# Kernel optimization log

Measured on AMD Instinct MI355X. Metric: run time of the kernel, lower is better.

The kernel has to match this reference:

```python
import jax
import jax.numpy as jnp
from jax import lax
import numpy as np

EPS = 1e-5
CLASS_COUNT = 1000

# conv specs: (out_c, in_c, k, pool_stride)
_SPECS = [(8, 1, 11, 1), (32, 8, 7, 2), (64, 32, 5, 2), (64, 64, 5, 2), (128, 64, 5, 2), (128, 128, 3, 2)]


def _maxpool3(x, stride):
    return lax.reduce_window(x, -jnp.inf, lax.max, (1, 1, 3, 3), (1, 1, stride, stride), 'VALID')


def _block(x, w, gamma, beta, pool_stride):
    # tanh soft-binarized weights (mode=1, w=1)
    wq = jnp.tanh(w)
    y = lax.conv_general_dilated(x, wq, (1, 1), 'VALID', dimension_numbers=('NCHW', 'OIHW', 'NCHW'))
    y = _maxpool3(y, pool_stride)
    # BatchNorm2d in training mode: batch statistics over (N,H,W), biased var
    mu = jnp.mean(y, axis=(0, 2, 3), keepdims=True)
    var = jnp.var(y, axis=(0, 2, 3), keepdims=True)
    y = (y - mu) * lax.rsqrt(var + EPS)
    y = y * gamma.reshape(1, -1, 1, 1) + beta.reshape(1, -1, 1, 1)
    # tanh soft-binarized activation (mode=1, w=1)
    return jnp.tanh(y)


def setup_inputs() -> dict:
    key = jax.random.key(0)
    keys = jax.random.split(key, 8)
    inp = {'x': jax.random.normal(keys[0], (128, 1, 227, 227), dtype=jnp.float32)}
    for i, (oc, ic, k, _) in enumerate(_SPECS):
        fan_in = ic * k * k
        inp[f'w{i+1}'] = jax.random.normal(keys[i + 1], (oc, ic, k, k), dtype=jnp.float32) / np.sqrt(fan_in)
        inp[f'g{i+1}'] = jnp.ones((oc,), dtype=jnp.float32)
        inp[f'b{i+1}'] = jnp.zeros((oc,), dtype=jnp.float32)
    inp['wl'] = jax.random.normal(keys[7], (CLASS_COUNT, 512), dtype=jnp.float32) / np.sqrt(512.0)
    return inp


def reference(x, w1, w2, w3, w4, w5, w6, g1, g2, g3, g4, g5, g6,
              b1, b2, b3, b4, b5, b6, wl):
    ws = (w1, w2, w3, w4, w5, w6)
    gs = (g1, g2, g3, g4, g5, g6)
    bs = (b1, b2, b3, b4, b5, b6)
    for i, (_, _, _, ps) in enumerate(_SPECS):
        x = _block(x, ws[i], gs[i], bs[i], ps)
    # flatten -> BinaryLinear (tanh-binarized weight, no bias)
    x = x.reshape(x.shape[0], -1)  # [B, 512]
    return x @ jnp.tanh(wl).T  # [B, classCount]
```

## Files before the change

kernel.cpp:

```cpp
#include <hip/hip_runtime.h>
#include <hip/hip_bf16.h>
#include <hip/hip_fp16.h>

using bf16 = __hip_bfloat16;
using f16  = _Float16;
using f16x8 = __attribute__((ext_vector_type(8))) _Float16;
using f32x4  = __attribute__((ext_vector_type(4))) float;
typedef unsigned long long u64;

__device__ __forceinline__ float b2f(bf16 v){ return __bfloat162float(v); }
__device__ __forceinline__ bf16 f2b(float v){ return __float2bfloat16(v); }
__device__ __forceinline__ float ldf(const float* p){ return *p; }
__device__ __forceinline__ float ldf(const bf16* p){ return b2f(*p); }
__device__ __forceinline__ float ldf(const __half* p){ return __half2float(*p); }
__device__ __forceinline__ void stf(float* p, float v){ *p = v; }
__device__ __forceinline__ void stf(bf16* p, float v){ *p = f2b(v); }
__device__ __forceinline__ void stf(__half* p, float v){ *p = __float2half(v); }

__device__ __forceinline__ float ftanh(float x){
    float t = __builtin_amdgcn_exp2f(x * 2.8853900817779268f);
    return 1.0f - 2.0f * __builtin_amdgcn_rcpf(t + 1.0f);
}

__device__ __forceinline__ float ld_any(const void* p, int i, int isBf16)
{
    return isBf16 ? b2f(((const bf16*)p)[i]) : ((const float*)p)[i];
}

__device__ __forceinline__ int det_bf(const void* g)
{
    return (*(const unsigned*)g == 0x3F803F80u) ? 1 : 0;
}

__device__ __forceinline__ void bn_pr(const float* __restrict__ sums,
                                      const void* __restrict__ g,
                                      const void* __restrict__ b,
                                      int bf, int C, float inv, int c,
                                      float& sc, float& sh)
{
    float mean = sums[c] * inv;
    float var  = sums[C + c] * inv - mean * mean;
    float rstd = rsqrtf(fmaxf(var, 0.f) + 1e-5f);
    sc = ld_any(g, c, bf) * rstd;
    sh = ld_any(b, c, bf) - mean * sc;
}

__global__ __launch_bounds__(256)
void prep_all(const void* __restrict__ w1, const void* __restrict__ w6,
              const void* __restrict__ wlw, const void* __restrict__ w2,
              const void* __restrict__ w3, const void* __restrict__ w4,
              const void* __restrict__ w5, const void* __restrict__ g1,
              float* __restrict__ wq0, float* __restrict__ wq5,
              float* __restrict__ wlqT, __half* __restrict__ wpk,
              __half* __restrict__ wpk3, __half* __restrict__ wpk4,
              __half* __restrict__ wpk5, int* __restrict__ flag)
{
    const int bf = det_bf(g1);
    const int b = blockIdx.x, t = threadIdx.x;
    if (b == 0 && t == 0) *flag = bf;
    if (b < 4) {
        int i = b * 256 + t;
        if (i < 968) wq0[i] = tanhf(ld_any(w1, i, bf));
    } else if (b < 580) {
        int i = (b - 4) * 256 + t;
        if (i < 147456) wq5[i] = tanhf(ld_any(w6, i, bf));
    } else if (b < 2580) {
        int i = (b - 580) * 256 + t;
        if (i < 512000) {
            int cls = i >> 9, k = i & 511;
            wlqT[k * 1000 + cls] = tanhf(ld_any(wlw, i, bf));
        }
    } else if (b < 2636) {
        int i = (b - 2580) * 256 + t;
        if (i < 14336) {
            int ic  = i & 7;
            int q   = (i >> 3) & 3;
            int col = (i >> 5) & 15;
            int g   = (i >> 9) & 1;
            int khg = (i >> 10) & 1;
            int kw  = i >> 11;
            int kh  = khg * 4 + q;
            int oc  = g * 16 + col;
            __half v = __float2half(0.f);
            if (kh < 7)
                v = __float2half(tanhf(ld_any(w2, (oc * 8 + ic) * 49 + kh * 7 + kw, bf)));
            wpk[i] = v;
        }
    } else if (b < 2836) {
        int i = (b - 2636) * 256 + t;
        if (i < 51200) {
            int tap = i >> 11;
            int g   = (i >> 9) & 3;
            int col = (i >> 5) & 15;
            int icp = i & 31;
            int oc  = g * 16 + col;
            wpk3[i] = __float2half(tanhf(ld_any(w3, (oc * 32 + icp) * 25 + tap, bf)));
        }
    } else if (b < 3236) {
        int i = (b - 2836) * 256 + t;
        if (i < 102400) {
            int step = i >> 11;
            int g    = (i >> 9) & 3;
            int col  = (i >> 5) & 15;
            int icp  = i & 31;
            int icg  = step / 25, tap = step - icg * 25;
            int oc   = g * 16 + col;
            int ic   = icg * 32 + icp;
            wpk4[i] = __float2half(tanhf(ld_any(w4, (oc * 64 + ic) * 25 + tap, bf)));
        }
    } else {
        int i = (b - 3236) * 256 + t;
        if (i < 204800) {
            int step = i >> 12;
            int ocg  = (i >> 11) & 1;
            int g    = (i >> 9) & 3;
            int col  = (i >> 5) & 15;
            int icp  = i & 31;
            int icg  = step / 25, tap = step - icg * 25;
            int oc   = ocg * 64 + g * 16 + col;
            int ic   = icg * 32 + icp;
            wpk5[i] = __float2half(tanhf(ld_any(w5, (oc * 64 + ic) * 25 + tap, bf)));
        }
    }
}

__global__ __launch_bounds__(256)
void b2conv(const __half* __restrict__ A1, const __half* __restrict__ wpk,
            __half* __restrict__ raw, float* __restrict__ sums2,
            const float* __restrict__ sums1, const void* __restrict__ g1,
            const void* __restrict__ b1)
{
    __shared__ __align__(16) char smem[32000];
    __shared__ float s_part[512];
    f16*   xs = (f16*)smem;
    float* pb = (float*)smem;

    const int tid = threadIdx.x;
    const int n   = blockIdx.z;
    const int ty  = blockIdx.x / 15, tx = blockIdx.x - ty * 15;
    const int cy0 = ty * 30, cx0 = tx * 14;

    const int bf1 = det_bf(g1);
    float ssc[8], ssh[8];
    #pragma unroll
    for (int j = 0; j < 8; j++)
        bn_pr(sums1, g1, b1, bf1, 8, 1.f / 5916800.f, j, ssc[j], ssh[j]);

    for (int i = tid; i < 858; i += 256) {
        int r = i / 22, c = i - r * 22;
        int gr = cy0 + r, gc = cx0 + c;
        f16x8 v = (f16x8){0, 0, 0, 0, 0, 0, 0, 0};
        if (gr < 215 && gc < 215)
            v = *(const f16x8*)((const f16*)A1 + ((size_t)(n * 215 + gr) * 215 + gc) * 8);
        f16x8 o;
        #pragma unroll
        for (int j = 0; j < 8; j++)
            o[j] = (f16)ftanh(fmaf((float)v[j], ssc[j], ssh[j]));
        *(f16x8*)(xs + i * 8) = o;
    }
    __syncthreads();

    const int lane = tid & 63, wid = tid >> 6;
    const int col = lane & 15, q = lane >> 4;
    const int arow = q * 22;

    f32x4 acc[8][2];
    #pragma unroll
    for (int f = 0; f < 8; f++)
        #pragma unroll
        for (int g = 0; g < 2; g++)
            acc[f][g] = (f32x4){0.f, 0.f, 0.f, 0.f};

    const f16* wb = (const f16*)wpk + col * 32 + q * 8;
    f16x8 wc0 = *(const f16x8*)(wb);
    f16x8 wc1 = *(const f16x8*)(wb + 512);

    #pragma unroll
    for (int s = 0; s < 14; s++) {
        f16x8 wn0 = wc0, wn1 = wc1;
        if (s < 13) {
            const f16* wn = wb + (s + 1) * 1024;
            wn0 = *(const f16x8*)(wn);
            wn1 = *(const f16x8*)(wn + 512);
        }
        int kw = s >> 1, khg = s & 1;
        int aoffs = arow + khg * 88 + kw;
        #pragma unroll
        for (int f = 0; f < 8; f++) {
            int gi = (wid * 8 + f) * 22 + col + aoffs;
            f16x8 a = *(const f16x8*)(xs + gi * 8);
            acc[f][0] = __builtin_amdgcn_mfma_f32_16x16x32_f16(a, wc0, acc[f][0], 0, 0, 0);
            acc[f][1] = __builtin_amdgcn_mfma_f32_16x16x32_f16(a, wc1, acc[f][1], 0, 0, 0);
        }
        wc0 = wn0; wc1 = wn1;
    }
    __syncthreads();

    for (int h = 0; h < 2; h++) {
        #pragma unroll
        for (int f = 0; f < 8; f++) {
            int cr = wid * 8 + f;
            if (cr < 31)
                *(f32x4*)(pb + col * 500 + cr * 16 + q * 4) = acc[f][h];
        }
        __syncthreads();
        const int ocl = tid >> 4, slot = tid & 15;
        float sm = 0.f, sq = 0.f;
        for (int j = slot; j < 105; j += 16) {
            int py = j / 7, px = j - (j / 7) * 7;
            int gph = ty * 15 + py, gpw = tx * 7 + px;
            if (gph < 104 && gpw < 104) {
                const float* cp = pb + ocl * 500 + (2 * py) * 16 + 2 * px;
                float m = cp[0];
                #pragma unroll
                for (int dy = 0; dy < 3; dy++)
                    #pragma unroll
                    for (int dx = 0; dx < 3; dx++)
                        m = fmaxf(m, cp[dy * 16 + dx]);
                int oc = h * 16 + ocl;
                size_t oidx = ((size_t)(n * 104 + gph) * 104 + gpw) * 32 + oc;
                raw[oidx] = __float2half(m);
                sm += m; sq += m * m;
            }
        }
        s_part[tid] = sm; s_part[256 + tid] = sq;
        __syncthreads();
        if (tid < 16) {
            float a = 0.f, b = 0.f;
            #pragma unroll
            for (int t = 0; t < 16; t++) {
                a += s_part[tid * 16 + t];
                b += s_part[256 + tid * 16 + t];
            }
            atomicAdd(&sums2[h * 16 + tid],      a);
            atomicAdd(&sums2[32 + h * 16 + tid], b);
        }
        __syncthreads();
    }
}

__global__ __launch_bounds__(256)
void b3conv(const __half* __restrict__ A2, const __half* __restrict__ wpk3,
            __half* __restrict__ A3t, float* __restrict__ sums3,
            const float* __restrict__ sums2, const void* __restrict__ g2,
            const void* __restrict__ b2)
{
    __shared__ __align__(16) char smem[32000];
    __shared__ float s_part[512];
    f16*   xs = (f16*)smem;
    float* pb = (float*)smem;

    const int tid = threadIdx.x;
    const int n   = blockIdx.z;
    const int ty  = blockIdx.x / 7, tx = blockIdx.x - ty * 7;
    const int y0  = ty * 14, x0 = tx * 14;

    if (tid < 32) {
        float sc, sh;
        bn_pr(sums2, g2, b2, det_bf(g2), 32, 1.f / 1384448.f, tid, sc, sh);
        s_part[tid] = sc; s_part[32 + tid] = sh;
    }
    __syncthreads();

    for (int i = tid; i < 1600; i += 256) {
        int pos = i >> 2, g8 = i & 3;
        int gy = y0 + pos / 20, gx = x0 + pos % 20;
        f16x8 v = *(const f16x8*)((const f16*)A2 +
                  ((size_t)(n * 104 + gy) * 104 + gx) * 32 + g8 * 8);
        int c0 = g8 * 8;
        f16x8 o;
        #pragma unroll
        for (int j = 0; j < 8; j++)
            o[j] = (f16)ftanh(fmaf((float)v[j], s_part[c0 + j], s_part[32 + c0 + j]));
        *(f16x8*)(xs + pos * 40 + g8 * 8) = o;
    }

    const int lane = tid & 63, wid = tid >> 6;
    const int col = lane & 15, q = lane >> 4;

    f32x4 acc[4][4];
    #pragma unroll
    for (int f = 0; f < 4; f++)
        #pragma unroll
        for (int g = 0; g < 4; g++)
            acc[f][g] = (f32x4){0.f, 0.f, 0.f, 0.f};

    const f16* wb = (const f16*)wpk3 + col * 32 + q * 8;
    f16x8 w[4];
    #pragma unroll
    for (int g = 0; g < 4; g++)
        w[g] = *(const f16x8*)(wb + g * 512);

    __syncthreads();

    #pragma unroll 1
    for (int tap = 0; tap < 25; tap++) {
        const f16* wnb = wb + (tap < 24 ? tap + 1 : tap) * 2048;
        f16x8 wn[4];
        #pragma unroll
        for (int g = 0; g < 4; g++)
            wn[g] = *(const f16x8*)(wnb + g * 512);

        int kh = tap / 5, kw = tap - (tap / 5) * 5;
        f16x8 a[4];
        #pragma unroll
        for (int f = 0; f < 4; f++) {
            int pos = (wid * 4 + f + kh) * 20 + col + kw;
            a[f] = *(const f16x8*)(xs + pos * 40 + q * 8);
        }
        #pragma unroll
        for (int g = 0; g < 4; g++)
            #pragma unroll
            for (int f = 0; f < 4; f++)
                acc[f][g] = __builtin_amdgcn_mfma_f32_16x16x32_f16(
                    a[f], w[g], acc[f][g], 0, 0, 0);
        #pragma unroll
        for (int g = 0; g < 4; g++)
            w[g] = wn[g];
    }

    for (int h = 0; h < 2; h++) {
        __syncthreads();
        #pragma unroll
        for (int f = 0; f < 4; f++) {
            int cr = wid * 4 + f;
            if (cr < 15) {
                #pragma unroll
                for (int gg = 0; gg < 2; gg++)
                    *(f32x4*)(pb + (gg * 16 + col) * 244 + cr * 16 + q * 4) = acc[f][h * 2 + gg];
            }
        }
        __syncthreads();
        const int ocl = tid >> 3, slot = tid & 7;
        float sm = 0.f, sq = 0.f;
        for (int j = slot; j < 49; j += 8) {
            int py = j / 7, px = j - (j / 7) * 7;
            const float* cp = pb + ocl * 244 + (2 * py) * 16 + 2 * px;
            float m = cp[0];
            #pragma unroll
            for (int dy = 0; dy < 3; dy++)
                #pragma unroll
                for (int dx = 0; dx < 3; dx++)
                    m = fmaxf(m, cp[dy * 16 + dx]);
            int gph = ty * 7 + py, gpw = tx * 7 + px;
            A3t[((size_t)(n * 49 + gph) * 49 + gpw) * 64 + h * 32 + ocl]
                = __float2half(m);
            sm += m; sq += m * m;
        }
        s_part[tid] = sm; s_part[256 + tid] = sq;
        __syncthreads();
        if (tid < 32) {
            float a = 0.f, b = 0.f;
            #pragma unroll
            for (int t = 0; t < 8; t++) {
                a += s_part[tid * 8 + t];
                b += s_part[256 + tid * 8 + t];
            }
            atomicAdd(&sums3[h * 32 + tid],      a);
            atomicAdd(&sums3[64 + h * 32 + tid], b);
        }
    }
}

__global__ __launch_bounds__(256)
void b4conv(const __half* __restrict__ A3t, const __half* __restrict__ wpk4,
            __half* __restrict__ A4, float* __restrict__ sums4,
            const float* __restrict__ sums3, const void* __restrict__ g3,
            const void* __restrict__ b3)
{
    __shared__ __align__(16) char smem[31232];
    __shared__ float s_part[512];
    __shared__ float s_ss[128];
    f16*   xs = (f16*)smem;
    float* pb = (float*)smem;

    const int tid = threadIdx.x;
    const int n   = blockIdx.z;
    const int ty  = blockIdx.x >> 2, tx = blockIdx.x & 3;
    const int y0  = ty * 14, x0 = tx * 14;
    const int lane = tid & 63, wid = tid >> 6;
    const int col = lane & 15, q = lane >> 4;

    if (tid < 64) {
        float sc, sh;
        bn_pr(sums3, g3, b3, det_bf(g3), 64, 1.f / 307328.f, tid, sc, sh);
        s_ss[tid] = sc; s_ss[64 + tid] = sh;
    }

    f32x4 acc[4][4];
    #pragma unroll
    for (int f = 0; f < 4; f++)
        #pragma unroll
        for (int g = 0; g < 4; g++)
            acc[f][g] = (f32x4){0.f, 0.f, 0.f, 0.f};

    const f16* wb = (const f16*)wpk4 + col * 32 + q * 8;
    f16x8 w[4];
    #pragma unroll
    for (int g = 0; g < 4; g++)
        w[g] = *(const f16x8*)(wb + g * 512);

    #pragma unroll 1
    for (int icg = 0; icg < 2; icg++) {
        __syncthreads();
        for (int i = tid; i < 1520; i += 256) {
            int pos = i >> 2, g8 = i & 3;
            int gy = y0 + pos / 20, gx = x0 + pos % 20;
            f16x8 o = (f16x8){0, 0, 0, 0, 0, 0, 0, 0};
            if (gy < 49 && gx < 49) {
                f16x8 v = *(const f16x8*)((const f16*)A3t +
                    ((size_t)(n * 49 + gy) * 49 + gx) * 64 + icg * 32 + g8 * 8);
                int c0 = icg * 32 + g8 * 8;
                #pragma unroll
                for (int j = 0; j < 8; j++)
                    o[j] = (f16)ftanh(fmaf((float)v[j], s_ss[c0 + j], s_ss[64 + c0 + j]));
            }
            *(f16x8*)(xs + pos * 40 + g8 * 8) = o;
        }
        __syncthreads();

        #pragma unroll 1
        for (int tap = 0; tap < 25; tap++) {
            int step = icg * 25 + tap;
            const f16* wnb = wb + (size_t)(step < 49 ? step + 1 : step) * 2048;
            f16x8 wn[4];
            #pragma unroll
            for (int g = 0; g < 4; g++)
                wn[g] = *(const f16x8*)(wnb + g * 512);

            int kh = tap / 5, kw = tap - (tap / 5) * 5;
            f16x8 a[4];
            #pragma unroll
            for (int f = 0; f < 4; f++) {
                int r = wid * 4 + f + kh; if (r > 18) r = 18;
                int pos = r * 20 + col + kw;
                a[f] = *(const f16x8*)(xs + pos * 40 + q * 8);
            }
            #pragma unroll
            for (int g = 0; g < 4; g++)
                #pragma unroll
                for (int f = 0; f < 4; f++)
                    acc[f][g] = __builtin_amdgcn_mfma_f32_16x16x32_f16(
                        a[f], w[g], acc[f][g], 0, 0, 0);
            #pragma unroll
            for (int g = 0; g < 4; g++)
                w[g] = wn[g];
        }
    }

    for (int h = 0; h < 2; h++) {
        __syncthreads();
        #pragma unroll
        for (int f = 0; f < 4; f++) {
            int cr = wid * 4 + f;
            if (cr < 15) {
                #pragma unroll
                for (int gg = 0; gg < 2; gg++)
                    *(f32x4*)(pb + (gg * 16 + col) * 244 + cr * 16 + q * 4) = acc[f][h * 2 + gg];
            }
        }
        __syncthreads();
        const int ocl = tid >> 3, slot = tid & 7;
        float sm = 0.f, sq = 0.f;
        for (int j = slot; j < 49; j += 8) {
            int py = j / 7, px = j - (j / 7) * 7;
            int gph = ty * 7 + py, gpw = tx * 7 + px;
            if (gph < 22 && gpw < 22) {
                const float* cp = pb + ocl * 244 + (2 * py) * 16 + 2 * px;
                float m = cp[0];
                #pragma unroll
                for (int dy = 0; dy < 3; dy++)
                    #pragma unroll
                    for (int dx = 0; dx < 3; dx++)
                        m = fmaxf(m, cp[dy * 16 + dx]);
                A4[((size_t)(n * 22 + gph) * 22 + gpw) * 64 + h * 32 + ocl]
                    = __float2half(m);
                sm += m; sq += m * m;
            }
        }
        s_part[tid] = sm; s_part[256 + tid] = sq;
        __syncthreads();
        if (tid < 32) {
            float a = 0.f, b = 0.f;
            #pragma unroll
            for (int t = 0; t < 8; t++) {
                a += s_part[tid * 8 + t];
                b += s_part[256 + tid * 8 + t];
            }
            atomicAdd(&sums4[h * 32 + tid],      a);
            atomicAdd(&sums4[64 + h * 32 + tid], b);
        }
    }
}

__global__ __launch_bounds__(256)
void b5conv(const __half* __restrict__ A4, const __half* __restrict__ wpk5,
            float* __restrict__ A5, float* __restrict__ sums5,
            const float* __restrict__ sums4, const void* __restrict__ g4,
            const void* __restrict__ b4)
{
    __shared__ __align__(16) char smem[49664];
    __shared__ float s_part[512];
    __shared__ float s_ss[128];
    f16*   xs = (f16*)smem;
    float* pb = (float*)smem;

    const int tid = threadIdx.x;
    const int n   = blockIdx.z;
    const int ocg = blockIdx.x;
    const int lane = tid & 63, wid = tid >> 6;
    const int col = lane & 15, q = lane >> 4;

    if (tid < 64) {
        float sc, sh;
        bn_pr(sums4, g4, b4, det_bf(g4), 64, 1.f / 61952.f, tid, sc, sh);
        s_ss[tid] = sc; s_ss[64 + tid] = sh;
    }

    int abase[6];
    #pragma unroll
    for (int f = 0; f < 6; f++) {
        int m = (wid * 6 + f) * 16 + col;
        if (m > 323) m = 323;
        int r = m / 18, cc = m - r * 18;
        abase[f] = r * 22 + cc;
    }

    f32x4 acc[6][4];
    #pragma unroll
    for (int f = 0; f < 6; f++)
        #pragma unroll
        for (int g = 0; g < 4; g++)
            acc[f][g] = (f32x4){0.f, 0.f, 0.f, 0.f};

    const f16* wb = (const f16*)wpk5 + ocg * 2048 + col * 32 + q * 8;
    f16x8 w[4];
    #pragma unroll
    for (int g = 0; g < 4; g++)
        w[g] = *(const f16x8*)(wb + g * 512);

    #pragma unroll 1
    for (int icg = 0; icg < 2; icg++) {
        __syncthreads();
        for (int i = tid; i < 1936; i += 256) {
            int pos = i >> 2, g8 = i & 3;
            f16x8 v = *(const f16x8*)((const f16*)A4 + ((size_t)(n * 484 + pos)) * 64
                                      + icg * 32 + g8 * 8);
            int c0 = icg * 32 + g8 * 8;
            f16x8 o;
            #pragma unroll
            for (int j = 0; j < 8; j++)
                o[j] = (f16)ftanh(fmaf((float)v[j], s_ss[c0 + j], s_ss[64 + c0 + j]));
            *(f16x8*)(xs + pos * 40 + g8 * 8) = o;
        }
        __syncthreads();

        #pragma unroll 1
        for (int tap = 0; tap < 25; tap++) {
            int step = icg * 25 + tap;
            const f16* wnb = wb + (size_t)(step < 49 ? step + 1 : step) * 4096;
            f16x8 wn[4];
            #pragma unroll
            for (int g = 0; g < 4; g++)
                wn[g] = *(const f16x8*)(wnb + g * 512);

            int kh = tap / 5, kw = tap - (tap / 5) * 5;
            int off = kh * 22 + kw;
            f16x8 a[6];
            #pragma unroll
            for (int f = 0; f < 6; f++)
                a[f] = *(const f16x8*)(xs + (abase[f] + off) * 40 + q * 8);
            #pragma unroll
            for (int g = 0; g < 4; g++)
                #pragma unroll
                for (int f = 0; f < 6; f++)
                    acc[f][g] = __builtin_amdgcn_mfma_f32_16x16x32_f16(
                        a[f], w[g], acc[f][g], 0, 0, 0);
            #pragma unroll
            for (int g = 0; g < 4; g++)
                w[g] = wn[g];
        }
    }

    for (int h = 0; h < 2; h++) {
        __syncthreads();
        #pragma unroll
        for (int f = 0; f < 6; f++)
            #pragma unroll
            for (int gg = 0; gg < 2; gg++)
                *(f32x4*)(pb + (gg * 16 + col) * 388 + (wid * 6 + f) * 16 + q * 4)
                    = acc[f][h * 2 + gg];
        __syncthreads();
        const int ocl = tid >> 3, slot = tid & 7;
        float sm = 0.f, sq = 0.f;
        for (int j = slot; j < 64; j += 8) {
            int py = j >> 3, px = j & 7;
            const float* cp = pb + ocl * 388 + (2 * py) * 18 + 2 * px;
            float m = cp[0];
            #pragma unroll
            for (int dy = 0; dy < 3; dy++)
                #pragma unroll
                for (int dx = 0; dx < 3; dx++)
                    m = fmaxf(m, cp[dy * 18 + dx]);
            int oc = ocg * 64 + h * 32 + ocl;
            A5[((size_t)(n * 128 + oc) * 8 + py) * 8 + px] = m;
            sm += m; sq += m * m;
        }
        s_part[tid] = sm; s_part[256 + tid] = sq;
        __syncthreads();
        if (tid < 32) {
            float a = 0.f, b = 0.f;
            #pragma unroll
            for (int t = 0; t < 8; t++) {
                a += s_part[tid * 8 + t];
                b += s_part[256 + tid * 8 + t];
            }
            int oc = ocg * 64 + h * 32 + tid;
            atomicAdd(&sums5[oc],       a);
            atomicAdd(&sums5[128 + oc], b);
        }
    }
}

template<int MODE, int RAWIN, int IC, int OC, int K, int PS, int TPH, int TPW,
         int OCB, int OCT, int CIC, int NP, bool ONHWC, typename InT, typename OutT>
__global__ __launch_bounds__(256)
void ctile(const void* __restrict__ in, const float* __restrict__ wq,
           OutT* __restrict__ out, float* __restrict__ sums,
           const float* __restrict__ ss, const void* __restrict__ g1in,
           int Hin, int Win, int PH, int PW, int tilesX)
{
    constexpr int TPO  = OCB / OCT;
    constexpr int CH   = PS * (TPH - 1) + 3;
    constexpr int CW   = PS * (TPW - 1) + 3;
    constexpr int SPR  = (CW + NP - 1) / NP;
    constexpr int CWP  = SPR * NP;
    constexpr int NSTR = CH * SPR;
    static_assert(NSTR * TPO <= 256, "thread mapping overflow");
    constexpr int IH   = CH + K - 1;
    constexpr int IW   = CW + K - 1;
    constexpr int IWE_ = (CWP + K - 1 > IW) ? (CWP + K - 1) : IW;
    constexpr int IWE  = IWE_ | 1;
    constexpr int IN_SZ  = CIC * IH * IWE;
    constexpr int INP    = (IN_SZ + 3) & ~3;
    constexpr int W_SZ   = CIC * K * K * OCB;
    constexpr int CONV_SZ = OCB * CH * CWP;
    constexpr int LDS_SZ = (INP + W_SZ > CONV_SZ) ? (INP + W_SZ) : CONV_SZ;

    __shared__ __align__(16) float lds[LDS_SZ];
    __shared__ float s_part[512];

    const int tid = threadIdx.x;
    const int n   = blockIdx.z;
    const int oc0 = blockIdx.y * OCB;
    const int tY  = blockIdx.x / tilesX;
    const int tX  = blockIdx.x - tY * tilesX;
    const int ph0 = tY * TPH, pw0 = tX * TPW;
    const int ih0 = ph0 * PS, iw0 = pw0 * PS;

    const int bfin = RAWIN ? det_bf(g1in) : 0;

    const int  og  = tid % TPO;
    const int  s   = tid / TPO;
    const bool act = (s < NSTR);
    const int  r   = s / SPR;
    const int  c0  = (s - r * SPR) * NP;

    float acc[NP][OCT];
    #pragma unroll
    for (int p = 0; p < NP; p++)
        #pragma unroll
        for (int o = 0; o < OCT; o++) acc[p][o] = 0.f;

    for (int icb = 0; icb < IC; icb += CIC) {
        for (int idx = tid; idx < IN_SZ; idx += 256) {
            int ic  = idx / (IH * IWE);
            int rem = idx - ic * (IH * IWE);
            int rr  = rem / IWE, cc = rem - rr * IWE;
            int gr  = ih0 + rr, gc = iw0 + cc;
            float v = 0.f;
            if (gr < Hin && gc < Win) {
                size_t gidx = ((size_t)(n * IC + icb + ic) * Hin + gr) * Win + gc;
                v = RAWIN ? ld_any(in, (int)gidx, bfin) : ldf(&((const InT*)in)[gidx]);
            }
            lds[idx] = v;
        }
        for (int idx = tid; idx < W_SZ; idx += 256) {
            int ocl = idx % OCB;
            int kk  = (idx / OCB) % (K * K);
            int c_  = idx / (OCB * K * K);
            lds[INP + idx] = wq[((size_t)(oc0 + ocl) * IC + icb + c_) * (K * K) + kk];
        }
        __syncthreads();

        if (act) {
            #pragma unroll 1
            for (int ic_ = 0; ic_ < CIC; ic_++) {
                const float* xb = lds + ic_ * (IH * IWE);
                const float* wb = lds + INP + ic_ * (K * K * OCB) + og * OCT;
                #pragma unroll 1
                for (int kh = 0; kh < K; kh++) {
                    const float* xr = xb + (r + kh) * IWE + c0;
                    float xwin[NP + K - 1];
                    #pragma unroll
                    for (int j = 0; j < NP + K - 1; j++) xwin[j] = xr[j];
                    #pragma unroll
                    for (int kw = 0; kw < K; kw++) {
                        const float* wp2 = wb + (kh * K + kw) * OCB;
                        float wv[OCT];
                        #pragma unroll
                        for (int o = 0; o < OCT; o += 4) {
                            float4 t = *(const float4*)(wp2 + o);
                            wv[o] = t.x; wv[o+1] = t.y; wv[o+2] = t.z; wv[o+3] = t.w;
                        }
                        #pragma unroll
                        for (int p = 0; p < NP; p++)
                            #pragma unroll
                            for (int o = 0; o < OCT; o++)
                                acc[p][o] = fmaf(wv[o], xwin[p + kw], acc[p][o]);
                    }
                }
            }
        }
        __syncthreads();
    }

    if (act) {
        #pragma unroll
        for (int p = 0; p < NP; p++)
            #pragma unroll
            for (int o = 0; o < OCT; o++)
                lds[(og * OCT + o) * (CH * CWP) + r * CWP + c0 + p] = acc[p][o];
    }
    __syncthreads();

    {
        constexpr int TPC = 256 / OCB;
        const int ocl = tid / TPC, slot = tid - ocl * TPC;
        float sm = 0.f, sq = 0.f;
        for (int j = slot; j < TPH * TPW; j += TPC) {
            int py = j / TPW, px = j - (j / TPW) * TPW;
            int gph = ph0 + py, gpw = pw0 + px;
            if (gph < PH && gpw < PW) {
                const float* cp = lds + ocl * (CH * CWP) + (py * PS) * CWP + px * PS;
                float m = cp[0];
                #pragma unroll
                for (int dy = 0; dy < 3; dy++)
                    #pragma unroll
                    for (int dx = 0; dx < 3; dx++)
                        m = fmaxf(m, cp[dy * CWP + dx]);
                size_t oidx = ONHWC
                    ? ((size_t)(n * PH + gph) * PW + gpw) * OC + oc0 + ocl
                    : ((size_t)(n * OC + oc0 + ocl) * PH + gph) * PW + gpw;
                if (MODE == 2) {
                    int c = oc0 + ocl;
                    stf(&out[oidx], ftanh(fmaf(m, ss[c], ss[OC + c])));
                } else {
                    if (MODE == 0) stf(&out[oidx], m);
                    sm += m; sq += m * m;
                }
            }
        }
        if (MODE != 2) {
            s_part[tid] = sm; s_part[256 + tid] = sq;
            __syncthreads();
            if (tid < OCB) {
                float a = 0.f, b = 0.f;
                #pragma unroll
                for (int t = 0; t < TPC; t++) {
                    a += s_part[tid * TPC + t];
                    b += s_part[256 + tid * TPC + t];
                }
                atomicAdd(&sums[oc0 + tid],      a);
                atomicAdd(&sums[OC + oc0 + tid], b);
            }
        }
    }
}

template<int K, int APPLY, typename InT, typename OutT>
__global__ __launch_bounds__(256)
void convpool(const InT* __restrict__ in, const float* __restrict__ wq,
              OutT* __restrict__ out, const float* __restrict__ ss,
              int IC, int OC, int PS, int Hin, int Win, int PH, int PW, int total)
{
    for (int idx = blockIdx.x * 256 + threadIdx.x; idx < total;
         idx += gridDim.x * 256) {
        int pw = idx % PW;
        int t1 = idx / PW;
        int ph = t1 % PH;
        int t2 = t1 / PH;
        int oc = t2 % OC;
        int n  = t2 / OC;
        const int by = ph * PS, bx = pw * PS;

        float acc[3][3];
        #pragma unroll
        for (int a = 0; a < 3; a++)
            #pragma unroll
            for (int b = 0; b < 3; b++) acc[a][b] = 0.f;

        const float* wp = wq + oc * IC * K * K;
        const InT*   np = in + (n * IC) * Hin * Win;

        #pragma unroll 1
        for (int ic = 0; ic < IC; ic++) {
            const InT*   xp = np + ic * Hin * Win;
            const float* wc = wp + ic * K * K;
            #pragma unroll
            for (int r = 0; r < K + 2; r++) {
                float xr[K + 2];
                const InT* xrow = xp + (by + r) * Win + bx;
                #pragma unroll
                for (int j = 0; j < K + 2; j++) xr[j] = ldf(&xrow[j]);
                #pragma unroll
                for (int dy = 0; dy < 3; dy++) {
                    const int kh = r - dy;
                    if (0 <= kh && kh < K) {
                        const float* wrow = wc + kh * K;
                        #pragma unroll
                        for (int kw = 0; kw < K; kw++) {
                            float w = wrow[kw];
                            acc[dy][0] = fmaf(w, xr[kw + 0], acc[dy][0]);
                            acc[dy][1] = fmaf(w, xr[kw + 1], acc[dy][1]);
                            acc[dy][2] = fmaf(w, xr[kw + 2], acc[dy][2]);
                        }
                    }
                }
            }
        }
        float m = acc[0][0];
        #pragma unroll
        for (int a = 0; a < 3; a++)
            #pragma unroll
            for (int b = 0; b < 3; b++) m = fmaxf(m, acc[a][b]);
        if (APPLY) m = ftanh(fmaf(m, ss[oc], ss[OC + oc]));
        stf(&out[idx], m);
    }
}

template<typename T>
__global__ __launch_bounds__(256)
void stats_k(const T* __restrict__ x, float* __restrict__ sums,
             int N, int C, int PHW, int bpc)
{
    int c   = blockIdx.x / bpc;
    int sub = blockIdx.x % bpc;
    int perC = N * PHW;
    float s = 0.f, s2 = 0.f;
    for (int j = sub * 256 + threadIdx.x; j < perC; j += bpc * 256) {
        int n = j / PHW, p = j - n * PHW;
        float v = ldf(&x[(n * C + c) * PHW + p]);
        s += v; s2 += v * v;
    }
    __shared__ float ls[256], ls2[256];
    ls[threadIdx.x] = s; ls2[threadIdx.x] = s2;
    __syncthreads();
    for (int w = 128; w > 0; w >>= 1) {
        if (threadIdx.x < w) {
            ls[threadIdx.x]  += ls[threadIdx.x + w];
            ls2[threadIdx.x] += ls2[threadIdx.x + w];
        }
        __syncthreads();
    }
    if (threadIdx.x == 0) {
        atomicAdd(&sums[c],     ls[0]);
        atomicAdd(&sums[C + c], ls2[0]);
    }
}

__global__ __launch_bounds__(256)
void bn_tanh_p(float* __restrict__ x, const float* __restrict__ sums,
               const void* __restrict__ g, const void* __restrict__ b,
               int C, int PHW, float invCnt)
{
    int plane = blockIdx.y;
    int c = plane & (C - 1);
    float sc, sh;
    bn_pr(sums, g, b, det_bf(g), C, invCnt, c, sc, sh);
    float* xp = x + (long)plane * PHW;
    for (int i = blockIdx.x * 256 + threadIdx.x; i < PHW; i += 256 * gridDim.x)
        xp[i] = ftanh(fmaf(xp[i], sc, sh));
}

__global__ __launch_bounds__(256)
void linear_k(const float* __restrict__ act, const float* __restrict__ wlqT,
              void* __restrict__ out, const int* __restrict__ flag)
{
    __shared__ float s_a[512];
    int bf = *flag;
    int n = blockIdx.y;
    for (int i = threadIdx.x; i < 512; i += 256) s_a[i] = act[n * 512 + i];
    __syncthreads();
    int cls = blockIdx.x * 256 + threadIdx.x;
    if (cls < 1000) {
        float acc = 0.f;
        #pragma unroll 8
        for (int k = 0; k < 512; k++)
            acc = fmaf(s_a[k], wlqT[k * 1000 + cls], acc);
        if (bf) ((bf16*)out)[n * 1000 + cls] = f2b(acc);
        else    ((float*)out)[n * 1000 + cls] = acc;
    }
}

extern "C" void kernel_launch(void* const* d_in, const int* in_sizes, int n_in,
                              void* d_out, int out_size, void* d_ws, size_t ws_size,
                              hipStream_t stream)
{
    (void)in_sizes; (void)n_in; (void)out_size; (void)ws_size;
    const void* x = d_in[0];
    const void* W[6]; const void* G[6]; const void* B[6];
    for (int i = 0; i < 6; i++) {
        W[i] = d_in[1 + 3 * i];
        G[i] = d_in[2 + 3 * i];
        B[i] = d_in[3 + 3 * i];
    }
    const void* wl = d_in[19];

    char* p = (char*)d_ws;
    auto carve = [&](size_t bytes) -> void* {
        void* r = (void*)p;
        p += (bytes + 255) & ~((size_t)255);
        return r;
    };
    int*   flag = (int*)carve(256);
    const int wsz[6] = {968, 12544, 51200, 102400, 204800, 147456};
    float* wq[6];
    for (int i = 0; i < 6; i++) wq[i] = (float*)carve((size_t)wsz[i] * 4);
    float* wlqT = (float*)carve((size_t)512000 * 4);
    float* sums_all = (float*)carve(1536 * 4);
    float* S1 = sums_all;        float* S2 = sums_all + 256;
    float* S3 = sums_all + 512;  float* S4 = sums_all + 768;
    float* S5 = sums_all + 1024; float* S6 = sums_all + 1280;
    __half* wpk  = (__half*)carve((size_t)14336 * 2);
    __half* wpk3 = (__half*)carve((size_t)51200 * 2);
    __half* wpk4 = (__half*)carve((size_t)102400 * 2);
    __half* wpk5 = (__half*)carve((size_t)204800 * 2);
    __half* R1  = (__half*)carve((size_t)47334400 * 2);
    __half* R2  = (__half*)carve((size_t)44302336 * 2);
    __half* A1  = R1;
    __half* A2  = R2;
    __half* A3t = R1;
    __half* A4  = R2;
    float*  A5  = (float*)R1;
    float*  A6  = (float*)R2;

    auto cdiv = [](int a, int b) { return (a + b - 1) / b; };

    hipMemsetAsync(sums_all, 0, 1536 * 4, stream);
    prep_all<<<4036, 256, 0, stream>>>(W[0], W[5], wl, W[1], W[2], W[3], W[4], G[0],
                                       wq[0], wq[5], wlqT, wpk, wpk3, wpk4, wpk5, flag);

    ctile<0, 1, 1, 8, 11, 1, 34, 40, 8, 8, 1, 7, true, float, __half>
        <<<dim3(42, 1, 128), 256, 0, stream>>>(x, wq[0], A1, S1, S1, G[0], 227, 227, 215, 215, 6);

    b2conv<<<dim3(105, 1, 128), 256, 0, stream>>>(A1, wpk, A2, S2, S1, G[0], B[0]);

    b3conv<<<dim3(49, 1, 128), 256, 0, stream>>>(A2, wpk3, A3t, S3, S2, G[1], B[1]);

    b4conv<<<dim3(16, 1, 128), 256, 0, stream>>>(A3t, wpk4, A4, S4, S3, G[2], B[2]);

    b5conv<<<dim3(2, 1, 128), 256, 0, stream>>>(A4, wpk5, A5, S5, S4, G[3], B[3]);
    bn_tanh_p<<<dim3(1, 16384), 256, 0, stream>>>(A5, S5, G[4], B[4], 128, 64, 1.f / 8192.f);

    {
        int total = 65536;
        convpool<3, 0, float, float><<<cdiv(total, 256), 256, 0, stream>>>(
            A5, wq[5], A6, S6, 128, 128, 2, 8, 8, 2, 2, total);
        stats_k<float><<<128, 256, 0, stream>>>(A6, S6, 128, 128, 4, 1);
        bn_tanh_p<<<dim3(1, 16384), 256, 0, stream>>>(A6, S6, G[5], B[5], 128, 4, 1.f / 512.f);
    }
    linear_k<<<dim3(4, 128), 256, 0, stream>>>(A6, wlqT, d_out, flag);
}
```

Baseline: 1.305 ms.

## Fuse tail-stage stats and BN-tanh into conv6 and linear kernels

Replaces the per-plane BN-tanh launch for block 5 with a flat elementwise kernel that uses far fewer blocks than the old 16384-block grid. The block-6 conv now computes its batch statistics in-kernel through wave shuffles and atomics, which removes the separate stats kernel. The block-6 BN and tanh are folded into the linear kernel's activation load, which removes another launch and a pass over the data. The cost is that each linear block recomputes the 128 per-channel scale and shift values, and more atomics go to the sums buffer.

```diff
diff --git a/kernel.cpp b/kernel.cpp
--- a/kernel.cpp
+++ b/kernel.cpp
@@ -619,6 +619,85 @@
             atomicAdd(&sums5[oc],       a);
             atomicAdd(&sums5[128 + oc], b);
         }
+    }
+}
+
+__global__ __launch_bounds__(256)
+void bn_tanh_flat(float* __restrict__ x, const float* __restrict__ sums,
+                  const void* __restrict__ g, const void* __restrict__ b, int n)
+{
+    int idx = blockIdx.x * 256 + threadIdx.x;
+    if (idx >= n) return;
+    int c = (idx >> 6) & 127;
+    float sc, sh;
+    bn_pr(sums, g, b, det_bf(g), 128, 1.f / 8192.f, c, sc, sh);
+    x[idx] = ftanh(fmaf(x[idx], sc, sh));
+}
+
+template<int K>
+__global__ __launch_bounds__(256)
+void convpool_s(const float* __restrict__ in, const float* __restrict__ wq,
+                float* __restrict__ out, float* __restrict__ sums,
+                int IC, int OC, int PS, int Hin, int Win, int PH, int PW, int total)
+{
+    int idx = blockIdx.x * 256 + threadIdx.x;
+    if (idx >= total) return;
+    int pw = idx % PW;
+    int t1 = idx / PW;
+    int ph = t1 % PH;
+    int t2 = t1 / PH;
+    int oc = t2 % OC;
+    int n  = t2 / OC;
+    const int by = ph * PS, bx = pw * PS;
+
+    float acc[3][3];
+    #pragma unroll
+    for (int a = 0; a < 3; a++)
+        #pragma unroll
+        for (int b = 0; b < 3; b++) acc[a][b] = 0.f;
+
+    const float* wp = wq + oc * IC * K * K;
+    const float* np = in + (n * IC) * Hin * Win;
+
+    #pragma unroll 1
+    for (int ic = 0; ic < IC; ic++) {
+        const float* xp = np + ic * Hin * Win;
+        const float* wc = wp + ic * K * K;
+        #pragma unroll
+        for (int r = 0; r < K + 2; r++) {
+            float xr[K + 2];
+            const float* xrow = xp + (by + r) * Win + bx;
+            #pragma unroll
+            for (int j = 0; j < K + 2; j++) xr[j] = xrow[j];
+            #pragma unroll
+            for (int dy = 0; dy < 3; dy++) {
+                const int kh = r - dy;
+                if (0 <= kh && kh < K) {
+                    const float* wrow = wc + kh * K;
+                    #pragma unroll
+                    for (int kw = 0; kw < K; kw++) {
+                        float w = wrow[kw];
+                        acc[dy][0] = fmaf(w, xr[kw + 0], acc[dy][0]);
+                        acc[dy][1] = fmaf(w, xr[kw + 1], acc[dy][1]);
+                        acc[dy][2] = fmaf(w, xr[kw + 2], acc[dy][2]);
+                    }
+                }
+            }
+        }
+    }
+    float m = acc[0][0];
+    #pragma unroll
+    for (int a = 0; a < 3; a++)
+        #pragma unroll
+        for (int b = 0; b < 3; b++) m = fmaxf(m, acc[a][b]);
+    out[idx] = m;
+
+    float s1 = m, s2 = m * m;
+    s1 += __shfl_xor(s1, 1); s2 += __shfl_xor(s2, 1);
+    s1 += __shfl_xor(s1, 2); s2 += __shfl_xor(s2, 2);
+    if ((threadIdx.x & 3) == 0) {
+        atomicAdd(&sums[oc],      s1);
+        atomicAdd(&sums[OC + oc], s2);
     }
 }
 
@@ -778,121 +857,29 @@
     }
 }
 
-template<int K, int APPLY, typename InT, typename OutT>
-__global__ __launch_bounds__(256)
-void convpool(const InT* __restrict__ in, const float* __restrict__ wq,
-              OutT* __restrict__ out, const float* __restrict__ ss,
-              int IC, int OC, int PS, int Hin, int Win, int PH, int PW, int total)
-{
-    for (int idx = blockIdx.x * 256 + threadIdx.x; idx < total;
-         idx += gridDim.x * 256) {
-        int pw = idx % PW;
-        int t1 = idx / PW;
-        int ph = t1 % PH;
-        int t2 = t1 / PH;
-        int oc = t2 % OC;
-        int n  = t2 / OC;
-        const int by = ph * PS, bx = pw * PS;
-
-        float acc[3][3];
-        #pragma unroll
-        for (int a = 0; a < 3; a++)
-            #pragma unroll
-            for (int b = 0; b < 3; b++) acc[a][b] = 0.f;
-
-        const float* wp = wq + oc * IC * K * K;
-        const InT*   np = in + (n * IC) * Hin * Win;
-
-        #pragma unroll 1
-        for (int ic = 0; ic < IC; ic++) {
-            const InT*   xp = np + ic * Hin * Win;
-            const float* wc = wp + ic * K * K;
-            #pragma unroll
-            for (int r = 0; r < K + 2; r++) {
-                float xr[K + 2];
-                const InT* xrow = xp + (by + r) * Win + bx;
-                #pragma unroll
-                for (int j = 0; j < K + 2; j++) xr[j] = ldf(&xrow[j]);
-                #pragma unroll
-                for (int dy = 0; dy < 3; dy++) {
-                    const int kh = r - dy;
-                    if (0 <= kh && kh < K) {
-                        const float* wrow = wc + kh * K;
-                        #pragma unroll
-                        for (int kw = 0; kw < K; kw++) {
-                            float w = wrow[kw];
-                            acc[dy][0] = fmaf(w, xr[kw + 0], acc[dy][0]);
-                            acc[dy][1] = fmaf(w, xr[kw + 1], acc[dy][1]);
-                            acc[dy][2] = fmaf(w, xr[kw + 2], acc[dy][2]);
-                        }
-                    }
-                }
-            }
-        }
-        float m = acc[0][0];
-        #pragma unroll
-        for (int a = 0; a < 3; a++)
-            #pragma unroll
-            for (int b = 0; b < 3; b++) m = fmaxf(m, acc[a][b]);
-        if (APPLY) m = ftanh(fmaf(m, ss[oc], ss[OC + oc]));
-        stf(&out[idx], m);
-    }
-}
-
-template<typename T>
-__global__ __launch_bounds__(256)
-void stats_k(const T* __restrict__ x, float* __restrict__ sums,
-             int N, int C, int PHW, int bpc)
-{
-    int c   = blockIdx.x / bpc;
-    int sub = blockIdx.x % bpc;
-    int perC = N * PHW;
-    float s = 0.f, s2 = 0.f;
-    for (int j = sub * 256 + threadIdx.x; j < perC; j += bpc * 256) {
-        int n = j / PHW, p = j - n * PHW;
-        float v = ldf(&x[(n * C + c) * PHW + p]);
-        s += v; s2 += v * v;
-    }
-    __shared__ float ls[256], ls2[256];
-    ls[threadIdx.x] = s; ls2[threadIdx.x] = s2;
-    __syncthreads();
-    for (int w = 128; w > 0; w >>= 1) {
-        if (threadIdx.x < w) {
-            ls[threadIdx.x]  += ls[threadIdx.x + w];
-            ls2[threadIdx.x] += ls2[threadIdx.x + w];
-        }
-        __syncthreads();
-    }
-    if (threadIdx.x == 0) {
-        atomicAdd(&sums[c],     ls[0]);
-        atomicAdd(&sums[C + c], ls2[0]);
-    }
-}
-
-__global__ __launch_bounds__(256)
-void bn_tanh_p(float* __restrict__ x, const float* __restrict__ sums,
-               const void* __restrict__ g, const void* __restrict__ b,
-               int C, int PHW, float invCnt)
-{
-    int plane = blockIdx.y;
-    int c = plane & (C - 1);
-    float sc, sh;
-    bn_pr(sums, g, b, det_bf(g), C, invCnt, c, sc, sh);
-    float* xp = x + (long)plane * PHW;
-    for (int i = blockIdx.x * 256 + threadIdx.x; i < PHW; i += 256 * gridDim.x)
-        xp[i] = ftanh(fmaf(xp[i], sc, sh));
-}
-
 __global__ __launch_bounds__(256)
 void linear_k(const float* __restrict__ act, const float* __restrict__ wlqT,
-              void* __restrict__ out, const int* __restrict__ flag)
+              void* __restrict__ out, const int* __restrict__ flag,
+              const float* __restrict__ sums6, const void* __restrict__ g6,
+              const void* __restrict__ b6)
 {
     __shared__ float s_a[512];
+    __shared__ float s_ss[256];
     int bf = *flag;
+    int tid = threadIdx.x;
+    if (tid < 128) {
+        float sc, sh;
+        bn_pr(sums6, g6, b6, bf, 128, 1.f / 512.f, tid, sc, sh);
+        s_ss[tid] = sc; s_ss[128 + tid] = sh;
+    }
+    __syncthreads();
     int n = blockIdx.y;
-    for (int i = threadIdx.x; i < 512; i += 256) s_a[i] = act[n * 512 + i];
+    for (int i = tid; i < 512; i += 256) {
+        int c = i >> 2;
+        s_a[i] = ftanh(fmaf(act[n * 512 + i], s_ss[c], s_ss[128 + c]));
+    }
     __syncthreads();
-    int cls = blockIdx.x * 256 + threadIdx.x;
+    int cls = blockIdx.x * 256 + tid;
     if (cls < 1000) {
         float acc = 0.f;
         #pragma unroll 8
@@ -961,14 +948,10 @@
     b4conv<<<dim3(16, 1, 128), 256, 0, stream>>>(A3t, wpk4, A4, S4, S3, G[2], B[2]);
 
     b5conv<<<dim3(2, 1, 128), 256, 0, stream>>>(A4, wpk5, A5, S5, S4, G[3], B[3]);
-    bn_tanh_p<<<dim3(1, 16384), 256, 0, stream>>>(A5, S5, G[4], B[4], 128, 64, 1.f / 8192.f);
-
-    {
-        int total = 65536;
-        convpool<3, 0, float, float><<<cdiv(total, 256), 256, 0, stream>>>(
-            A5, wq[5], A6, S6, 128, 128, 2, 8, 8, 2, 2, total);
-        stats_k<float><<<128, 256, 0, stream>>>(A6, S6, 128, 128, 4, 1);
-        bn_tanh_p<<<dim3(1, 16384), 256, 0, stream>>>(A6, S6, G[5], B[5], 128, 4, 1.f / 512.f);
-    }
-    linear_k<<<dim3(4, 128), 256, 0, stream>>>(A6, wlqT, d_out, flag);
-}
+    bn_tanh_flat<<<cdiv(1048576, 256), 256, 0, stream>>>(A5, S5, G[4], B[4], 1048576);
+
+    convpool_s<3><<<cdiv(65536, 256), 256, 0, stream>>>(
+        A5, wq[5], A6, S6, 128, 128, 2, 8, 8, 2, 2, 65536);
+
+    linear_k<<<dim3(4, 128), 256, 0, stream>>>(A6, wlqT, d_out, flag, S6, G[5], B[5]);
+}
```

Result: faster. 1.274 ms, median of 2 (-2.4%).
